# Kernel tuning notes

Hardware: AMD Instinct MI355X
Metric: run time of the kernel (lower is better)

The kernel has to match this reference:

```python
import math
import jax, jax.numpy as jnp
import numpy as np

B, S, D = 4, 2048, 1024
EPS_LN = 1e-5
EPS_MAS = 1e-9


def layernorm(x, g, b):
    m = jnp.mean(x, axis=-1, keepdims=True)
    v = jnp.mean(jnp.square(x - m), axis=-1, keepdims=True)
    return (x - m) * jax.lax.rsqrt(v + EPS_LN) * g + b


def spl(x, proto_w, mu_w, mu_b, gate):
    # match_values = x @ proto^T / sqrt(d);  comp = silu(x @ mu^T + b)
    match = jnp.einsum('bsd,od->bso', x, proto_w) / math.sqrt(x.shape[-1])
    comp = jax.nn.silu(jnp.einsum('bsd,od->bso', x, mu_w) + mu_b)
    return comp, match, gate


def branch(comp, match, gate, passthrough):
    # mas_normalize on the 1-D gate vector (cost), broadcast over [B,S,D]
    cost = gate / (jnp.max(jnp.abs(gate)) + EPS_MAS)
    rl = match - cost
    mrl = jax.nn.relu(rl)
    mask = (rl > 0).astype(comp.dtype)
    return comp * mrl + passthrough * (1.0 - mask)


def causal_attention(q, k, v):
    # num_heads = 1, head_dim = D, is_causal=True
    scale = 1.0 / math.sqrt(q.shape[-1])
    scores = jnp.einsum('bqd,bkd->bqk', q, k) * scale
    causal = jnp.tril(jnp.ones((q.shape[1], k.shape[1]), dtype=bool))
    scores = jnp.where(causal, scores, jnp.asarray(-1e9, scores.dtype))
    p = jax.nn.softmax(scores, axis=-1)
    return jnp.einsum('bqk,bkd->bqd', p, v)


def setup_inputs() -> dict:
    key = jax.random.key(0)
    ks = jax.random.split(key, 16)
    d = D
    std = 0.02
    inp = {
        'x': jax.random.normal(ks[0], (B, S, d), jnp.float32),
        'ln_g': jnp.ones((d,), jnp.float32),
        'ln_b': jnp.zeros((d,), jnp.float32),
    }
    names = ['q', 'k', 'v', 'o']
    for i, n in enumerate(names):
        inp[f'{n}_mu_w'] = std * jax.random.normal(ks[1 + 3 * i], (d, d), jnp.float32)
        inp[f'{n}_mu_b'] = jnp.zeros((d,), jnp.float32)
        inp[f'{n}_proto'] = std * jax.random.normal(ks[2 + 3 * i], (d, d), jnp.float32)
        inp[f'{n}_gate'] = 0.1 * jax.random.normal(ks[3 + 3 * i], (d,), jnp.float32)
    return inp


def reference(x, ln_g, ln_b,
              q_mu_w, q_mu_b, q_proto, q_gate,
              k_mu_w, k_mu_b, k_proto, k_gate,
              v_mu_w, v_mu_b, v_proto, v_gate,
              o_mu_w, o_mu_b, o_proto, o_gate):
    ln1_out = layernorm(x, ln_g, ln_b)

    c_q, mv_q, g_q = spl(ln1_out, q_proto, q_mu_w, q_mu_b, q_gate)
    c_k, mv_k, g_k = spl(ln1_out, k_proto, k_mu_w, k_mu_b, k_gate)
    c_v, mv_v, g_v = spl(ln1_out, v_proto, v_mu_w, v_mu_b, v_gate)

    q = branch(c_q, mv_q, g_q, ln1_out)
    k = branch(c_k, mv_k, g_k, ln1_out)
    v = branch(c_v, mv_v, g_v, ln1_out)

    attn_out = causal_attention(q, k, v)

    c_o, mv_o, g_o = spl(attn_out, o_proto, o_mu_w, o_mu_b, o_gate)
    masked_o = branch(c_o, mv_o, g_o, attn_out)

    x_out = x + masked_o
    return x_out
```

## Files before the change

### kernel.cpp

```cpp
#include <hip/hip_runtime.h>
#include <hip/hip_bf16.h>
#include <cmath>
#include <cstdint>

typedef _Float16 f16;
typedef _Float16 f16x8 __attribute__((ext_vector_type(8)));
typedef float f32x4 __attribute__((ext_vector_type(4)));

#define D_ 1024
#define S_ 2048


__device__ __forceinline__ void gload_lds16(const void* g, void* l) {
  __builtin_amdgcn_global_load_lds(
      (const __attribute__((address_space(1))) void*)(unsigned long long)(uintptr_t)g,
      (__attribute__((address_space(3))) void*)(unsigned int)(uintptr_t)l,
      16, 0, 0);
}

__device__ __forceinline__ int lds_off(int row, int cb) {
  return (row << 5) + ((cb ^ ((row >> 1) & 3)) << 3);
}

__device__ __forceinline__ void split1024(float v, f16& h, f16& l) {
  float s = v * 1024.f;
  h = (f16)s;
  l = (f16)(s - (float)h);
}

__device__ __forceinline__ void stage_tile(const f16* __restrict__ src, int ld,
                                           f16* lds, int wid, int lane) {
  const int r = (wid << 5) + (lane >> 2);
  const int c = (lane & 3) ^ ((r >> 1) & 3);
  const f16* g0 = src + (size_t)r * ld + (c << 3);
  gload_lds16(g0, lds + (wid << 10));
  gload_lds16(g0 + (size_t)(ld << 4), lds + (wid << 10) + 512);
}

__global__ __launch_bounds__(256) void convert_w(
    const float* __restrict__ s0, const float* __restrict__ s1,
    const float* __restrict__ s2, const float* __restrict__ s3,
    const float* __restrict__ s4, const float* __restrict__ s5,
    const float* __restrict__ s6, const float* __restrict__ s7,
    f16* __restrict__ dst) {
  const float* srcs[8] = {s0, s1, s2, s3, s4, s5, s6, s7};
  const float* sp = srcs[blockIdx.y];
  f16* hi = dst + (size_t)blockIdx.y * 2097152;
  f16* lo = hi + 1048576;
  const int i = (blockIdx.x * 256 + threadIdx.x) << 2;
  float4 f = *(const float4*)(sp + i);
  __align__(8) f16 h4[4], l4[4];
  split1024(f.x, h4[0], l4[0]); split1024(f.y, h4[1], l4[1]);
  split1024(f.z, h4[2], l4[2]); split1024(f.w, h4[3], l4[3]);
  *(uint2*)(hi + i) = *(uint2*)h4;
  *(uint2*)(lo + i) = *(uint2*)l4;
}

__global__ __launch_bounds__(256) void cost_k(
    const float* __restrict__ g0, const float* __restrict__ g1,
    const float* __restrict__ g2, const float* __restrict__ g3,
    float* __restrict__ cost) {
  const float* gp = blockIdx.x == 0 ? g0 : blockIdx.x == 1 ? g1
                   : blockIdx.x == 2 ? g2 : g3;
  const int t = threadIdx.x;
  float4 v = *(const float4*)(gp + (t << 2));
  float mx = fmaxf(fmaxf(fabsf(v.x), fabsf(v.y)), fmaxf(fabsf(v.z), fabsf(v.w)));
  for (int o = 32; o; o >>= 1) mx = fmaxf(mx, __shfl_xor(mx, o, 64));
  __shared__ float red[4];
  if ((t & 63) == 0) red[t >> 6] = mx;
  __syncthreads();
  mx = fmaxf(fmaxf(red[0], red[1]), fmaxf(red[2], red[3]));
  const float den = mx + 1e-9f;
  float4 o = {v.x / den, v.y / den, v.z / den, v.w / den};
  *(float4*)(cost + (blockIdx.x << 10) + (t << 2)) = o;
}

__global__ __launch_bounds__(256) void layernorm_k(
    const float* __restrict__ x, const float* __restrict__ g,
    const float* __restrict__ bta, f16* __restrict__ Lh, f16* __restrict__ Ll) {
  const int row = blockIdx.x, t = threadIdx.x;
  const float* xr = x + (size_t)row * D_;
  float4 v = *(const float4*)(xr + (t << 2));
  float s = v.x + v.y + v.z + v.w;
  float q = v.x * v.x + v.y * v.y + v.z * v.z + v.w * v.w;
  for (int o = 32; o; o >>= 1) { s += __shfl_xor(s, o, 64); q += __shfl_xor(q, o, 64); }
  __shared__ float red[8];
  const int wid = t >> 6;
  if ((t & 63) == 0) { red[wid] = s; red[4 + wid] = q; }
  __syncthreads();
  s = red[0] + red[1] + red[2] + red[3];
  q = red[4] + red[5] + red[6] + red[7];
  const float mean = s * (1.f / D_);
  const float var = q * (1.f / D_) - mean * mean;
  const float inv = 1.f / sqrtf(var + 1e-5f);
  float4 gv = *(const float4*)(g + (t << 2));
  float4 bv = *(const float4*)(bta + (t << 2));
  __align__(8) f16 h4[4], l4[4];
  split1024((v.x - mean) * inv * gv.x + bv.x, h4[0], l4[0]);
  split1024((v.y - mean) * inv * gv.y + bv.y, h4[1], l4[1]);
  split1024((v.z - mean) * inv * gv.z + bv.z, h4[2], l4[2]);
  split1024((v.w - mean) * inv * gv.w + bv.w, h4[3], l4[3]);
  const size_t off = (size_t)row * D_ + (t << 2);
  *(uint2*)(Lh + off) = *(uint2*)h4;
  *(uint2*)(Ll + off) = *(uint2*)l4;
}

#define MFMA16(a, b, c) __builtin_amdgcn_mfma_f32_16x16x32_f16((a), (b), (c), 0, 0, 0)

#define PH_CORE(N)                                                        \
    const f16x8 bph = *(const f16x8*)&bb[16384 + boff[N]];                \
    const f16x8 bpl = *(const f16x8*)&bb[20480 + boff[N]];                \
    const f16x8 bmh = *(const f16x8*)&bb[24576 + boff[N]];                \
    const f16x8 bml = *(const f16x8*)&bb[28672 + boff[N]];                \
    asm volatile("s_waitcnt lgkmcnt(0)" ::: "memory");                    \
    __builtin_amdgcn_sched_barrier(0);                                    \
    __builtin_amdgcn_s_setprio(1);                                        \
    _Pragma("unroll")                                                     \
    for (int m = 0; m < 4; ++m) {                                         \
      accP[m][N] = MFMA16(ah[m], bph, accP[m][N]);                        \
      accP[m][N] = MFMA16(ah[m], bpl, accP[m][N]);                        \
      accP[m][N] = MFMA16(al[m], bph, accP[m][N]);                        \
      accM[m][N] = MFMA16(ah[m], bmh, accM[m][N]);                        \
      accM[m][N] = MFMA16(ah[m], bml, accM[m][N]);                        \
      if (MUP == 3) accM[m][N] = MFMA16(al[m], bmh, accM[m][N]);          \
    }                                                                     \
    __builtin_amdgcn_s_setprio(0);                                        \
    asm volatile("s_barrier" ::: "memory");

#define DOPHASE_S(N, G0, L0, G1, L1)                                      \
  { gload_lds16((G0), (L0)); gload_lds16((G1), (L1)); PH_CORE(N) }

#define DOPHASE_N(N) { PH_CORE(N) }

template <int EPI, int MUP>
__global__ __launch_bounds__(512, 1) void dual_gemm_v3(
    const f16* __restrict__ Ah, const f16* __restrict__ Al,
    const f16* __restrict__ Wph, const f16* __restrict__ Wpl,
    const f16* __restrict__ Wmh, const f16* __restrict__ Wml,
    const float* __restrict__ bias, const float* __restrict__ cost,
    const f16* __restrict__ passh, const f16* __restrict__ passl,
    const float* __restrict__ xres, f16* __restrict__ outh,
    f16* __restrict__ outl, float* __restrict__ outf) {
  __shared__ __align__(16) f16 smem[65536];
  const int tid = threadIdx.x, wid = tid >> 6, lane = tid & 63;
  const int row0 = blockIdx.x << 8, col0 = blockIdx.y << 7;
  const int wr = (wid >> 1) << 6, wc = (wid & 1) << 6;
  const int arow = lane & 15, cbk = lane >> 4;

  const int sr = tid >> 2;
  const int sc = ((tid & 3) ^ ((sr >> 1) & 3)) << 3;
  const int wbase = wid << 9;

  const f16* pA0 = Ah + (size_t)(row0 + sr) * D_ + sc;
  const f16* pA1 = Ah + (size_t)(row0 + 128 + sr) * D_ + sc;
  const f16* pL0 = Al + (size_t)(row0 + sr) * D_ + sc;
  const f16* pL1 = Al + (size_t)(row0 + 128 + sr) * D_ + sc;
  const f16* pPh = Wph + (size_t)(col0 + sr) * D_ + sc;
  const f16* pPl = Wpl + (size_t)(col0 + sr) * D_ + sc;
  const f16* pMh = Wmh + (size_t)(col0 + sr) * D_ + sc;
  const f16* pMl = Wml + (size_t)(col0 + sr) * D_ + sc;

  const f32x4 zero = {0.f, 0.f, 0.f, 0.f};
  f32x4 accP[4][4], accM[4][4];
#pragma unroll
  for (int m = 0; m < 4; ++m)
#pragma unroll
    for (int n = 0; n < 4; ++n) { accP[m][n] = zero; accM[m][n] = zero; }

  int aoff[4], boff[4];
#pragma unroll
  for (int m = 0; m < 4; ++m) aoff[m] = lds_off(wr + m * 16 + arow, cbk);
#pragma unroll
  for (int n = 0; n < 4; ++n) boff[n] = lds_off(wc + n * 16 + arow, cbk);

  {
    f16* b = smem;
    gload_lds16(pA0, b + wbase);          gload_lds16(pA1, b + 4096 + wbase);
    gload_lds16(pL0, b + 8192 + wbase);   gload_lds16(pL1, b + 12288 + wbase);
    gload_lds16(pPh, b + 16384 + wbase);  gload_lds16(pPl, b + 20480 + wbase);
    gload_lds16(pMh, b + 24576 + wbase);  gload_lds16(pMl, b + 28672 + wbase);
  }

  int cur = 0;
  for (int t = 0; t < 32; ++t) {
    const f16* bb = smem + (cur << 15);
    f16* nb = smem + ((cur ^ 1) << 15);
    const int kn = (t < 31) ? ((t + 1) << 5) : 0;

    f16x8 ah[4], al[4];
    gload_lds16(pA0 + kn, nb + wbase);
    gload_lds16(pA1 + kn, nb + 4096 + wbase);
    asm volatile("s_waitcnt vmcnt(2)\n\ts_barrier" ::: "memory");
    __builtin_amdgcn_sched_barrier(0);
#pragma unroll
    for (int m = 0; m < 4; ++m) {
      ah[m] = *(const f16x8*)&bb[aoff[m]];
      al[m] = *(const f16x8*)&bb[8192 + aoff[m]];
    }
    DOPHASE_S(0, pL0 + kn, nb + 8192 + wbase, pL1 + kn, nb + 12288 + wbase)
    DOPHASE_S(1, pPh + kn, nb + 16384 + wbase, pPl + kn, nb + 20480 + wbase)
    DOPHASE_S(2, pMh + kn, nb + 24576 + wbase, pMl + kn, nb + 28672 + wbase)
    DOPHASE_N(3)
    cur ^= 1;
  }

#pragma unroll
  for (int m = 0; m < 4; ++m) {
    const int rb = row0 + wr + m * 16 + ((lane >> 4) << 2);
#pragma unroll
    for (int n = 0; n < 4; ++n) {
      const int col = col0 + wc + n * 16 + (lane & 15);
      const float cb2 = cost[col], bbv = bias[col];
#pragma unroll
      for (int j = 0; j < 4; ++j) {
        const size_t off = (size_t)(rb + j) * D_ + col;
        const float match = accP[m][n][j] * (1.f / 33554432.f);
        const float pre = accM[m][n][j] * (1.f / 1048576.f) + bbv;
        const float comp = pre / (1.f + expf(-pre));
        const float rl = match - cb2;
        float ov;
        if (rl > 0.f) ov = comp * rl;
        else ov = ((float)passh[off] + (float)passl[off]) * (1.f / 1024.f);
        if (EPI == 0) {
          f16 h, l; split1024(ov, h, l);
          outh[off] = h; outl[off] = l;
        } else {
          outf[off] = xres[off] + ov;
        }
      }
    }
  }
}

__global__ __launch_bounds__(256) void transpose_v(
    const f16* __restrict__ Vh, const f16* __restrict__ Vl,
    f16* __restrict__ VTh, f16* __restrict__ VTl) {
  const int iz = blockIdx.z, b = iz & 3;
  const f16* src = (iz >> 2) ? Vl : Vh;
  f16* dst = (iz >> 2) ? VTl : VTh;
  const int d0 = blockIdx.x << 6, s0 = blockIdx.y << 6;
  __shared__ f16 tl[64][65];
  const int c = threadIdx.x & 63, r4 = threadIdx.x >> 6;
  const f16* vb = src + (size_t)b * S_ * D_;
#pragma unroll
  for (int i = 0; i < 16; ++i) {
    const int sr = (r4 << 4) + i;
    tl[sr][c] = vb[(size_t)(s0 + sr) * D_ + d0 + c];
  }
  __syncthreads();
  f16* db = dst + (size_t)b * D_ * S_;
#pragma unroll
  for (int i = 0; i < 16; ++i) {
    const int dr = (r4 << 4) + i;
    db[(size_t)(d0 + dr) * S_ + s0 + c] = tl[c][dr];
  }
}

__global__ __launch_bounds__(256, 2) void scores_gemm(
    const f16* __restrict__ Qh, const f16* __restrict__ Ql,
    const f16* __restrict__ Kh, const f16* __restrict__ Kl,
    float* __restrict__ SC) {
  const int rt = blockIdx.x, ct = blockIdx.y, b = blockIdx.z;
  if (ct > rt) return;
  __shared__ __align__(16) f16 lQh[4096], lQl[4096], lKh[4096], lKl[4096];
  const int tid = threadIdx.x, wid = tid >> 6, lane = tid & 63;
  const int row0 = rt << 7, col0 = ct << 7;
  const int wr = (wid >> 1) << 6, wc = (wid & 1) << 6;
  const int arow = lane & 15, cb = lane >> 4;
  const f32x4 zero = {0.f, 0.f, 0.f, 0.f};
  f32x4 acc[4][4];
#pragma unroll
  for (int m = 0; m < 4; ++m)
#pragma unroll
    for (int n = 0; n < 4; ++n) acc[m][n] = zero;
  const f16* Qhb = Qh + ((size_t)b * S_ + row0) * D_;
  const f16* Qlb = Ql + ((size_t)b * S_ + row0) * D_;
  const f16* Khb = Kh + ((size_t)b * S_ + col0) * D_;
  const f16* Klb = Kl + ((size_t)b * S_ + col0) * D_;
  for (int k = 0; k < D_; k += 32) {
    stage_tile(Qhb + k, D_, lQh, wid, lane);
    stage_tile(Qlb + k, D_, lQl, wid, lane);
    stage_tile(Khb + k, D_, lKh, wid, lane);
    stage_tile(Klb + k, D_, lKl, wid, lane);
    __syncthreads();
    f16x8 bh[4], bl[4];
#pragma unroll
    for (int n = 0; n < 4; ++n) {
      const int bo = lds_off(wc + n * 16 + arow, cb);
      bh[n] = *(const f16x8*)&lKh[bo];
      bl[n] = *(const f16x8*)&lKl[bo];
    }
#pragma unroll
    for (int m = 0; m < 4; ++m) {
      const int ao = lds_off(wr + m * 16 + arow, cb);
      f16x8 ah = *(const f16x8*)&lQh[ao];
      f16x8 al = *(const f16x8*)&lQl[ao];
#pragma unroll
      for (int n = 0; n < 4; ++n) {
        acc[m][n] = __builtin_amdgcn_mfma_f32_16x16x32_f16(ah, bh[n], acc[m][n], 0, 0, 0);
        acc[m][n] = __builtin_amdgcn_mfma_f32_16x16x32_f16(ah, bl[n], acc[m][n], 0, 0, 0);
        acc[m][n] = __builtin_amdgcn_mfma_f32_16x16x32_f16(al, bh[n], acc[m][n], 0, 0, 0);
      }
    }
    __syncthreads();
  }
  float* scb = SC + (size_t)b * S_ * S_;
#pragma unroll
  for (int m = 0; m < 4; ++m) {
    const int rb = row0 + wr + m * 16 + ((lane >> 4) << 2);
#pragma unroll
    for (int n = 0; n < 4; ++n) {
      const int col = col0 + wc + n * 16 + (lane & 15);
#pragma unroll
      for (int j = 0; j < 4; ++j)
        scb[(size_t)(rb + j) * S_ + col] = acc[m][n][j] * (1.f / 33554432.f);
    }
  }
}

__global__ __launch_bounds__(256) void softmax_rows(float* __restrict__ SC) {
  const int r = blockIdx.x;
  const int s = r & 2047;
  float* rowf = SC + (size_t)r * S_;
  const int t = threadIdx.x, c0 = t << 3;
  float f[8];
  float4 u0 = *(const float4*)(rowf + c0);
  float4 u1 = *(const float4*)(rowf + c0 + 4);
  f[0] = u0.x; f[1] = u0.y; f[2] = u0.z; f[3] = u0.w;
  f[4] = u1.x; f[5] = u1.y; f[6] = u1.z; f[7] = u1.w;
  float mx = -3.0e38f;
#pragma unroll
  for (int j = 0; j < 8; ++j)
    if (c0 + j <= s) mx = fmaxf(mx, f[j]);
  for (int o = 32; o; o >>= 1) mx = fmaxf(mx, __shfl_xor(mx, o, 64));
  __shared__ float red[8];
  const int wid = t >> 6;
  if ((t & 63) == 0) red[wid] = mx;
  __syncthreads();
  mx = fmaxf(fmaxf(red[0], red[1]), fmaxf(red[2], red[3]));
  float e[8];
  float sum = 0.f;
#pragma unroll
  for (int j = 0; j < 8; ++j) {
    e[j] = (c0 + j <= s) ? expf(f[j] - mx) : 0.f;
    sum += e[j];
  }
  for (int o = 32; o; o >>= 1) sum += __shfl_xor(sum, o, 64);
  if ((t & 63) == 0) red[4 + wid] = sum;
  __syncthreads();
  sum = red[4] + red[5] + red[6] + red[7];
  f16* rowh = (f16*)rowf;
  __align__(16) f16 ph[8], pl[8];
#pragma unroll
  for (int j = 0; j < 8; ++j) {
    float p = (e[j] / sum) * 2048.f;
    ph[j] = (f16)p;
    pl[j] = (f16)(p - (float)ph[j]);
  }
  *(uint4*)(rowh + c0) = *(uint4*)ph;
  *(uint4*)(rowh + 2048 + c0) = *(uint4*)pl;
}

__global__ __launch_bounds__(256, 2) void pv_gemm(
    const f16* __restrict__ P, const f16* __restrict__ VTh,
    const f16* __restrict__ VTl, f16* __restrict__ Ath, f16* __restrict__ Atl) {
  const int rt = blockIdx.x, ct = blockIdx.y, b = blockIdx.z;
  __shared__ __align__(16) f16 lPh[4096], lPl[4096], lVh[4096], lVl[4096];
  const int tid = threadIdx.x, wid = tid >> 6, lane = tid & 63;
  const int row0 = rt << 7, col0 = ct << 7;
  const int wr = (wid >> 1) << 6, wc = (wid & 1) << 6;
  const int arow = lane & 15, cb = lane >> 4;
  const f32x4 zero = {0.f, 0.f, 0.f, 0.f};
  f32x4 acc[4][4];
#pragma unroll
  for (int m = 0; m < 4; ++m)
#pragma unroll
    for (int n = 0; n < 4; ++n) acc[m][n] = zero;
  const f16* Pb = P + ((size_t)b * S_ + row0) * 4096;
  const f16* Vhb = VTh + (size_t)b * D_ * S_ + (size_t)col0 * S_;
  const f16* Vlb = VTl + (size_t)b * D_ * S_ + (size_t)col0 * S_;
  const int kend = (rt + 1) << 7;
  for (int k = 0; k < kend; k += 32) {
    stage_tile(Pb + k, 4096, lPh, wid, lane);
    stage_tile(Pb + 2048 + k, 4096, lPl, wid, lane);
    stage_tile(Vhb + k, S_, lVh, wid, lane);
    stage_tile(Vlb + k, S_, lVl, wid, lane);
    __syncthreads();
    f16x8 bh[4], bl[4];
#pragma unroll
    for (int n = 0; n < 4; ++n) {
      const int bo = lds_off(wc + n * 16 + arow, cb);
      bh[n] = *(const f16x8*)&lVh[bo];
      bl[n] = *(const f16x8*)&lVl[bo];
    }
#pragma unroll
    for (int m = 0; m < 4; ++m) {
      const int ao = lds_off(wr + m * 16 + arow, cb);
      f16x8 ah = *(const f16x8*)&lPh[ao];
      f16x8 al = *(const f16x8*)&lPl[ao];
#pragma unroll
      for (int n = 0; n < 4; ++n) {
        acc[m][n] = __builtin_amdgcn_mfma_f32_16x16x32_f16(ah, bh[n], acc[m][n], 0, 0, 0);
        acc[m][n] = __builtin_amdgcn_mfma_f32_16x16x32_f16(ah, bl[n], acc[m][n], 0, 0, 0);
        acc[m][n] = __builtin_amdgcn_mfma_f32_16x16x32_f16(al, bh[n], acc[m][n], 0, 0, 0);
      }
    }
    __syncthreads();
  }
#pragma unroll
  for (int m = 0; m < 4; ++m) {
    const int rb = row0 + wr + m * 16 + ((lane >> 4) << 2);
#pragma unroll
    for (int n = 0; n < 4; ++n) {
      const int col = col0 + wc + n * 16 + (lane & 15);
#pragma unroll
      for (int j = 0; j < 4; ++j) {
        const float at = acc[m][n][j] * (1.f / 2097152.f);
        const size_t off = ((size_t)b * S_ + rb + j) * D_ + col;
        f16 h, l; split1024(at, h, l);
        Ath[off] = h; Atl[off] = l;
      }
    }
  }
}

extern "C" void kernel_launch(void* const* d_in, const int* in_sizes, int n_in,
                              void* d_out, int out_size, void* d_ws, size_t ws_size,
                              hipStream_t stream) {
  (void)in_sizes; (void)n_in; (void)out_size; (void)ws_size;
  const float* x      = (const float*)d_in[0];
  const float* ln_g   = (const float*)d_in[1];
  const float* ln_b   = (const float*)d_in[2];
  const float* q_mu_w = (const float*)d_in[3];
  const float* q_mu_b = (const float*)d_in[4];
  const float* q_pro  = (const float*)d_in[5];
  const float* q_gate = (const float*)d_in[6];
  const float* k_mu_w = (const float*)d_in[7];
  const float* k_mu_b = (const float*)d_in[8];
  const float* k_pro  = (const float*)d_in[9];
  const float* k_gate = (const float*)d_in[10];
  const float* v_mu_w = (const float*)d_in[11];
  const float* v_mu_b = (const float*)d_in[12];
  const float* v_pro  = (const float*)d_in[13];
  const float* v_gate = (const float*)d_in[14];
  const float* o_mu_w = (const float*)d_in[15];
  const float* o_mu_b = (const float*)d_in[16];
  const float* o_pro  = (const float*)d_in[17];
  const float* o_gate = (const float*)d_in[18];

  char* w = (char*)d_ws;
  f16* WB = (f16*)w;
  const size_t WS = 2097152;
  f16* Lh  = (f16*)(w + 33554432);
  f16* Ll  = (f16*)(w + 50331648);
  f16* Qh  = (f16*)(w + 67108864);
  f16* Ql  = (f16*)(w + 83886080);
  f16* Kh  = (f16*)(w + 100663296);
  f16* Kl  = (f16*)(w + 117440512);
  f16* VTh = (f16*)(w + 134217728);
  f16* VTl = (f16*)(w + 150994944);
  float* SC = (float*)(w + 167772160);
  float* COST = (float*)(w + 234881024);
  f16* Vh = (f16*)SC;
  f16* Vl = (f16*)(w + 184549376);
  f16* Ath = Qh;  f16* Atl = Ql;

  convert_w<<<dim3(1024, 8), 256, 0, stream>>>(
      q_pro, q_mu_w, k_pro, k_mu_w, v_pro, v_mu_w, o_pro, o_mu_w, WB);
  cost_k<<<4, 256, 0, stream>>>(q_gate, k_gate, v_gate, o_gate, COST);
  layernorm_k<<<8192, 256, 0, stream>>>(x, ln_g, ln_b, Lh, Ll);

  dual_gemm_v3<0, 3><<<dim3(32, 8), 512, 0, stream>>>(
      Lh, Ll, WB, WB + 1048576, WB + WS, WB + WS + 1048576,
      q_mu_b, COST, Lh, Ll, nullptr, Qh, Ql, nullptr);
  dual_gemm_v3<0, 3><<<dim3(32, 8), 512, 0, stream>>>(
      Lh, Ll, WB + 2 * WS, WB + 2 * WS + 1048576, WB + 3 * WS, WB + 3 * WS + 1048576,
      k_mu_b, COST + 1024, Lh, Ll, nullptr, Kh, Kl, nullptr);
  dual_gemm_v3<0, 3><<<dim3(32, 8), 512, 0, stream>>>(
      Lh, Ll, WB + 4 * WS, WB + 4 * WS + 1048576, WB + 5 * WS, WB + 5 * WS + 1048576,
      v_mu_b, COST + 2048, Lh, Ll, nullptr, Vh, Vl, nullptr);

  transpose_v<<<dim3(16, 32, 8), 256, 0, stream>>>(Vh, Vl, VTh, VTl);
  scores_gemm<<<dim3(16, 16, 4), 256, 0, stream>>>(Qh, Ql, Kh, Kl, SC);
  softmax_rows<<<8192, 256, 0, stream>>>(SC);
  pv_gemm<<<dim3(16, 8, 4), 256, 0, stream>>>((const f16*)SC, VTh, VTl, Ath, Atl);

  dual_gemm_v3<1, 2><<<dim3(32, 8), 512, 0, stream>>>(
      Ath, Atl, WB + 6 * WS, WB + 6 * WS + 1048576, WB + 7 * WS, WB + 7 * WS + 1048576,
      o_mu_b, COST + 3072, Ath, Atl, x, nullptr, nullptr, (float*)d_out);
}
```

Baseline: 678.9 us.

## Double-buffer B fragments in registers and drop per-phase barriers in dual GEMM

Restructures the dual GEMM main loop so B fragments for the next N sub-tile are read from LDS into registers while MFMAs for the current sub-tile run, using two alternating register sets. The four per-phase s_barrier / lgkmcnt(0) waits are replaced by a single vmcnt(0) plus barrier at the end of each k-iteration. MFMAs are regrouped into independent runs across m to lengthen the gap between dependent accumulator updates. In exchange, register pressure rises, and global prefetch for the next tile must now fully complete by the end of each iteration rather than being waited on partially.

```diff
diff --git a/kernel.cpp b/kernel.cpp
--- a/kernel.cpp
+++ b/kernel.cpp
@@ -107,33 +107,27 @@
 
 #define MFMA16(a, b, c) __builtin_amdgcn_mfma_f32_16x16x32_f16((a), (b), (c), 0, 0, 0)
 
-#define PH_CORE(N)                                                        \
-    const f16x8 bph = *(const f16x8*)&bb[16384 + boff[N]];                \
-    const f16x8 bpl = *(const f16x8*)&bb[20480 + boff[N]];                \
-    const f16x8 bmh = *(const f16x8*)&bb[24576 + boff[N]];                \
-    const f16x8 bml = *(const f16x8*)&bb[28672 + boff[N]];                \
-    asm volatile("s_waitcnt lgkmcnt(0)" ::: "memory");                    \
-    __builtin_amdgcn_sched_barrier(0);                                    \
-    __builtin_amdgcn_s_setprio(1);                                        \
-    _Pragma("unroll")                                                     \
-    for (int m = 0; m < 4; ++m) {                                         \
-      accP[m][N] = MFMA16(ah[m], bph, accP[m][N]);                        \
-      accP[m][N] = MFMA16(ah[m], bpl, accP[m][N]);                        \
-      accP[m][N] = MFMA16(al[m], bph, accP[m][N]);                        \
-      accM[m][N] = MFMA16(ah[m], bmh, accM[m][N]);                        \
-      accM[m][N] = MFMA16(ah[m], bml, accM[m][N]);                        \
-      if (MUP == 3) accM[m][N] = MFMA16(al[m], bmh, accM[m][N]);          \
-    }                                                                     \
-    __builtin_amdgcn_s_setprio(0);                                        \
-    asm volatile("s_barrier" ::: "memory");
-
-#define DOPHASE_S(N, G0, L0, G1, L1)                                      \
-  { gload_lds16((G0), (L0)); gload_lds16((G1), (L1)); PH_CORE(N) }
-
-#define DOPHASE_N(N) { PH_CORE(N) }
+#define MFMA_PHASE(N, BPH, BPL, BMH, BML)                                  \
+  __builtin_amdgcn_sched_barrier(0);                                       \
+  __builtin_amdgcn_s_setprio(1);                                           \
+  _Pragma("unroll") for (int m = 0; m < 4; ++m)                            \
+      accP[m][N] = MFMA16(ah[m], (BPH), accP[m][N]);                       \
+  _Pragma("unroll") for (int m = 0; m < 4; ++m)                            \
+      accP[m][N] = MFMA16(ah[m], (BPL), accP[m][N]);                       \
+  _Pragma("unroll") for (int m = 0; m < 4; ++m)                            \
+      accP[m][N] = MFMA16(al[m], (BPH), accP[m][N]);                       \
+  _Pragma("unroll") for (int m = 0; m < 4; ++m)                            \
+      accM[m][N] = MFMA16(ah[m], (BMH), accM[m][N]);                       \
+  _Pragma("unroll") for (int m = 0; m < 4; ++m)                            \
+      accM[m][N] = MFMA16(ah[m], (BML), accM[m][N]);                       \
+  if (MUP == 3) {                                                          \
+    _Pragma("unroll") for (int m = 0; m < 4; ++m)                          \
+        accM[m][N] = MFMA16(al[m], (BMH), accM[m][N]);                     \
+  }                                                                        \
+  __builtin_amdgcn_s_setprio(0);
 
 template <int EPI, int MUP>
-__global__ __launch_bounds__(512, 1) void dual_gemm_v3(
+__global__ __launch_bounds__(512, 1) void dual_gemm_v4(
     const f16* __restrict__ Ah, const f16* __restrict__ Al,
     const f16* __restrict__ Wph, const f16* __restrict__ Wpl,
     const f16* __restrict__ Wmh, const f16* __restrict__ Wml,
@@ -180,6 +174,9 @@
     gload_lds16(pPh, b + 16384 + wbase);  gload_lds16(pPl, b + 20480 + wbase);
     gload_lds16(pMh, b + 24576 + wbase);  gload_lds16(pMl, b + 28672 + wbase);
   }
+  asm volatile("s_waitcnt vmcnt(0)" ::: "memory");
+  __builtin_amdgcn_s_barrier();
+  __builtin_amdgcn_sched_barrier(0);
 
   int cur = 0;
   for (int t = 0; t < 32; ++t) {
@@ -188,19 +185,46 @@
     const int kn = (t < 31) ? ((t + 1) << 5) : 0;
 
     f16x8 ah[4], al[4];
-    gload_lds16(pA0 + kn, nb + wbase);
-    gload_lds16(pA1 + kn, nb + 4096 + wbase);
-    asm volatile("s_waitcnt vmcnt(2)\n\ts_barrier" ::: "memory");
-    __builtin_amdgcn_sched_barrier(0);
 #pragma unroll
     for (int m = 0; m < 4; ++m) {
       ah[m] = *(const f16x8*)&bb[aoff[m]];
       al[m] = *(const f16x8*)&bb[8192 + aoff[m]];
     }
-    DOPHASE_S(0, pL0 + kn, nb + 8192 + wbase, pL1 + kn, nb + 12288 + wbase)
-    DOPHASE_S(1, pPh + kn, nb + 16384 + wbase, pPl + kn, nb + 20480 + wbase)
-    DOPHASE_S(2, pMh + kn, nb + 24576 + wbase, pMl + kn, nb + 28672 + wbase)
-    DOPHASE_N(3)
+    f16x8 xph = *(const f16x8*)&bb[16384 + boff[0]];
+    f16x8 xpl = *(const f16x8*)&bb[20480 + boff[0]];
+    f16x8 xmh = *(const f16x8*)&bb[24576 + boff[0]];
+    f16x8 xml = *(const f16x8*)&bb[28672 + boff[0]];
+    f16x8 yph = *(const f16x8*)&bb[16384 + boff[1]];
+    f16x8 ypl = *(const f16x8*)&bb[20480 + boff[1]];
+    f16x8 ymh = *(const f16x8*)&bb[24576 + boff[1]];
+    f16x8 yml = *(const f16x8*)&bb[28672 + boff[1]];
+    gload_lds16(pA0 + kn, nb + wbase);
+    gload_lds16(pA1 + kn, nb + 4096 + wbase);
+    MFMA_PHASE(0, xph, xpl, xmh, xml)
+
+    xph = *(const f16x8*)&bb[16384 + boff[2]];
+    xpl = *(const f16x8*)&bb[20480 + boff[2]];
+    xmh = *(const f16x8*)&bb[24576 + boff[2]];
+    xml = *(const f16x8*)&bb[28672 + boff[2]];
+    gload_lds16(pL0 + kn, nb + 8192 + wbase);
+    gload_lds16(pL1 + kn, nb + 12288 + wbase);
+    MFMA_PHASE(1, yph, ypl, ymh, yml)
+
+    yph = *(const f16x8*)&bb[16384 + boff[3]];
+    ypl = *(const f16x8*)&bb[20480 + boff[3]];
+    ymh = *(const f16x8*)&bb[24576 + boff[3]];
+    yml = *(const f16x8*)&bb[28672 + boff[3]];
+    gload_lds16(pPh + kn, nb + 16384 + wbase);
+    gload_lds16(pPl + kn, nb + 20480 + wbase);
+    MFMA_PHASE(2, xph, xpl, xmh, xml)
+
+    gload_lds16(pMh + kn, nb + 24576 + wbase);
+    gload_lds16(pMl + kn, nb + 28672 + wbase);
+    MFMA_PHASE(3, yph, ypl, ymh, yml)
+
+    asm volatile("s_waitcnt vmcnt(0)" ::: "memory");
+    __builtin_amdgcn_s_barrier();
+    __builtin_amdgcn_sched_barrier(0);
     cur ^= 1;
   }
 
@@ -470,13 +494,13 @@
   cost_k<<<4, 256, 0, stream>>>(q_gate, k_gate, v_gate, o_gate, COST);
   layernorm_k<<<8192, 256, 0, stream>>>(x, ln_g, ln_b, Lh, Ll);
 
-  dual_gemm_v3<0, 3><<<dim3(32, 8), 512, 0, stream>>>(
+  dual_gemm_v4<0, 3><<<dim3(32, 8), 512, 0, stream>>>(
       Lh, Ll, WB, WB + 1048576, WB + WS, WB + WS + 1048576,
       q_mu_b, COST, Lh, Ll, nullptr, Qh, Ql, nullptr);
-  dual_gemm_v3<0, 3><<<dim3(32, 8), 512, 0, stream>>>(
+  dual_gemm_v4<0, 3><<<dim3(32, 8), 512, 0, stream>>>(
       Lh, Ll, WB + 2 * WS, WB + 2 * WS + 1048576, WB + 3 * WS, WB + 3 * WS + 1048576,
       k_mu_b, COST + 1024, Lh, Ll, nullptr, Kh, Kl, nullptr);
-  dual_gemm_v3<0, 3><<<dim3(32, 8), 512, 0, stream>>>(
+  dual_gemm_v4<0, 3><<<dim3(32, 8), 512, 0, stream>>>(
       Lh, Ll, WB + 4 * WS, WB + 4 * WS + 1048576, WB + 5 * WS, WB + 5 * WS + 1048576,
       v_mu_b, COST + 2048, Lh, Ll, nullptr, Vh, Vl, nullptr);
 
@@ -485,7 +509,7 @@
   softmax_rows<<<8192, 256, 0, stream>>>(SC);
   pv_gemm<<<dim3(16, 8, 4), 256, 0, stream>>>((const f16*)SC, VTh, VTl, Ath, Atl);
 
-  dual_gemm_v3<1, 2><<<dim3(32, 8), 512, 0, stream>>>(
+  dual_gemm_v4<1, 2><<<dim3(32, 8), 512, 0, stream>>>(
       Ath, Atl, WB + 6 * WS, WB + 6 * WS + 1048576, WB + 7 * WS, WB + 7 * WS + 1048576,
       o_mu_b, COST + 3072, Ath, Atl, x, nullptr, nullptr, (float*)d_out);
 }
```

Result: no change. 672.5 us (-1.0%).

## Double dual-GEMM block to 1024 threads with 4x4 wave grid and simplified pipeline

Applied to the files above, without the earlier changes.

The dual GEMM kernel now runs 16 waves per block instead of 8. Each wave computes a 64x32 tile rather than 64x64, so it holds half as many accumulators. The staged four-phase interleaving of global-to-LDS loads with MFMA phases is replaced by one bulk prefetch per k-step, followed by the full MFMA loop and a barrier. The aim is more latency hiding through extra waves and lower register pressure, at the cost of losing the fine-grained load/compute overlap and raising per-thread A-fragment loads relative to the compute done.

```diff
diff --git a/kernel.cpp b/kernel.cpp
--- a/kernel.cpp
+++ b/kernel.cpp
@@ -107,33 +107,8 @@
 
 #define MFMA16(a, b, c) __builtin_amdgcn_mfma_f32_16x16x32_f16((a), (b), (c), 0, 0, 0)
 
-#define PH_CORE(N)                                                        \
-    const f16x8 bph = *(const f16x8*)&bb[16384 + boff[N]];                \
-    const f16x8 bpl = *(const f16x8*)&bb[20480 + boff[N]];                \
-    const f16x8 bmh = *(const f16x8*)&bb[24576 + boff[N]];                \
-    const f16x8 bml = *(const f16x8*)&bb[28672 + boff[N]];                \
-    asm volatile("s_waitcnt lgkmcnt(0)" ::: "memory");                    \
-    __builtin_amdgcn_sched_barrier(0);                                    \
-    __builtin_amdgcn_s_setprio(1);                                        \
-    _Pragma("unroll")                                                     \
-    for (int m = 0; m < 4; ++m) {                                         \
-      accP[m][N] = MFMA16(ah[m], bph, accP[m][N]);                        \
-      accP[m][N] = MFMA16(ah[m], bpl, accP[m][N]);                        \
-      accP[m][N] = MFMA16(al[m], bph, accP[m][N]);                        \
-      accM[m][N] = MFMA16(ah[m], bmh, accM[m][N]);                        \
-      accM[m][N] = MFMA16(ah[m], bml, accM[m][N]);                        \
-      if (MUP == 3) accM[m][N] = MFMA16(al[m], bmh, accM[m][N]);          \
-    }                                                                     \
-    __builtin_amdgcn_s_setprio(0);                                        \
-    asm volatile("s_barrier" ::: "memory");
-
-#define DOPHASE_S(N, G0, L0, G1, L1)                                      \
-  { gload_lds16((G0), (L0)); gload_lds16((G1), (L1)); PH_CORE(N) }
-
-#define DOPHASE_N(N) { PH_CORE(N) }
-
 template <int EPI, int MUP>
-__global__ __launch_bounds__(512, 1) void dual_gemm_v3(
+__global__ __launch_bounds__(1024) void dual_gemm_v5(
     const f16* __restrict__ Ah, const f16* __restrict__ Al,
     const f16* __restrict__ Wph, const f16* __restrict__ Wpl,
     const f16* __restrict__ Wmh, const f16* __restrict__ Wml,
@@ -144,42 +119,41 @@
   __shared__ __align__(16) f16 smem[65536];
   const int tid = threadIdx.x, wid = tid >> 6, lane = tid & 63;
   const int row0 = blockIdx.x << 8, col0 = blockIdx.y << 7;
-  const int wr = (wid >> 1) << 6, wc = (wid & 1) << 6;
+  const int wr = (wid & 3) << 6;
+  const int wc = (wid >> 2) << 5;
   const int arow = lane & 15, cbk = lane >> 4;
 
-  const int sr = tid >> 2;
-  const int sc = ((tid & 3) ^ ((sr >> 1) & 3)) << 3;
-  const int wbase = wid << 9;
-
-  const f16* pA0 = Ah + (size_t)(row0 + sr) * D_ + sc;
-  const f16* pA1 = Ah + (size_t)(row0 + 128 + sr) * D_ + sc;
-  const f16* pL0 = Al + (size_t)(row0 + sr) * D_ + sc;
-  const f16* pL1 = Al + (size_t)(row0 + 128 + sr) * D_ + sc;
-  const f16* pPh = Wph + (size_t)(col0 + sr) * D_ + sc;
-  const f16* pPl = Wpl + (size_t)(col0 + sr) * D_ + sc;
-  const f16* pMh = Wmh + (size_t)(col0 + sr) * D_ + sc;
-  const f16* pMl = Wml + (size_t)(col0 + sr) * D_ + sc;
+  const int srow = tid >> 2;
+  const int scA = ((tid & 3) ^ ((srow >> 1) & 3)) << 3;
+  const int wrow = srow & 127;
+  const int scW = ((tid & 3) ^ ((wrow >> 1) & 3)) << 3;
+  const int wsel = tid >> 9;
+  const int dstA = wid << 9;
+  const int dstW = 16384 + (wid << 9);
+  const int dstW2 = 24576 + (wid << 9);
+
+  const f16* pAh = Ah + (size_t)(row0 + srow) * D_ + scA;
+  const f16* pAl = Al + (size_t)(row0 + srow) * D_ + scA;
+  const f16* pW1 = (wsel ? Wpl : Wph) + (size_t)(col0 + wrow) * D_ + scW;
+  const f16* pW2 = (wsel ? Wml : Wmh) + (size_t)(col0 + wrow) * D_ + scW;
 
   const f32x4 zero = {0.f, 0.f, 0.f, 0.f};
-  f32x4 accP[4][4], accM[4][4];
+  f32x4 accP[4][2], accM[4][2];
 #pragma unroll
   for (int m = 0; m < 4; ++m)
 #pragma unroll
-    for (int n = 0; n < 4; ++n) { accP[m][n] = zero; accM[m][n] = zero; }
-
-  int aoff[4], boff[4];
+    for (int n = 0; n < 2; ++n) { accP[m][n] = zero; accM[m][n] = zero; }
+
+  int aoff[4], boff[2];
 #pragma unroll
   for (int m = 0; m < 4; ++m) aoff[m] = lds_off(wr + m * 16 + arow, cbk);
 #pragma unroll
-  for (int n = 0; n < 4; ++n) boff[n] = lds_off(wc + n * 16 + arow, cbk);
-
-  {
-    f16* b = smem;
-    gload_lds16(pA0, b + wbase);          gload_lds16(pA1, b + 4096 + wbase);
-    gload_lds16(pL0, b + 8192 + wbase);   gload_lds16(pL1, b + 12288 + wbase);
-    gload_lds16(pPh, b + 16384 + wbase);  gload_lds16(pPl, b + 20480 + wbase);
-    gload_lds16(pMh, b + 24576 + wbase);  gload_lds16(pMl, b + 28672 + wbase);
-  }
+  for (int n = 0; n < 2; ++n) boff[n] = lds_off(wc + n * 16 + arow, cbk);
+
+  gload_lds16(pAh, smem + dstA);
+  gload_lds16(pAl, smem + 8192 + dstA);
+  gload_lds16(pW1, smem + dstW);
+  gload_lds16(pW2, smem + dstW2);
 
   int cur = 0;
   for (int t = 0; t < 32; ++t) {
@@ -187,20 +161,38 @@
     f16* nb = smem + ((cur ^ 1) << 15);
     const int kn = (t < 31) ? ((t + 1) << 5) : 0;
 
+    gload_lds16(pAh + kn, nb + dstA);
+    gload_lds16(pAl + kn, nb + 8192 + dstA);
+    gload_lds16(pW1 + kn, nb + dstW);
+    gload_lds16(pW2 + kn, nb + dstW2);
+    asm volatile("s_waitcnt vmcnt(4)\n\ts_barrier" ::: "memory");
+    __builtin_amdgcn_sched_barrier(0);
+
     f16x8 ah[4], al[4];
-    gload_lds16(pA0 + kn, nb + wbase);
-    gload_lds16(pA1 + kn, nb + 4096 + wbase);
-    asm volatile("s_waitcnt vmcnt(2)\n\ts_barrier" ::: "memory");
-    __builtin_amdgcn_sched_barrier(0);
 #pragma unroll
     for (int m = 0; m < 4; ++m) {
       ah[m] = *(const f16x8*)&bb[aoff[m]];
       al[m] = *(const f16x8*)&bb[8192 + aoff[m]];
     }
-    DOPHASE_S(0, pL0 + kn, nb + 8192 + wbase, pL1 + kn, nb + 12288 + wbase)
-    DOPHASE_S(1, pPh + kn, nb + 16384 + wbase, pPl + kn, nb + 20480 + wbase)
-    DOPHASE_S(2, pMh + kn, nb + 24576 + wbase, pMl + kn, nb + 28672 + wbase)
-    DOPHASE_N(3)
+    __builtin_amdgcn_s_setprio(1);
+#pragma unroll
+    for (int n = 0; n < 2; ++n) {
+      const f16x8 bph = *(const f16x8*)&bb[16384 + boff[n]];
+      const f16x8 bpl = *(const f16x8*)&bb[20480 + boff[n]];
+      const f16x8 bmh = *(const f16x8*)&bb[24576 + boff[n]];
+      const f16x8 bml = *(const f16x8*)&bb[28672 + boff[n]];
+#pragma unroll
+      for (int m = 0; m < 4; ++m) {
+        accP[m][n] = MFMA16(ah[m], bph, accP[m][n]);
+        accP[m][n] = MFMA16(ah[m], bpl, accP[m][n]);
+        accP[m][n] = MFMA16(al[m], bph, accP[m][n]);
+        accM[m][n] = MFMA16(ah[m], bmh, accM[m][n]);
+        accM[m][n] = MFMA16(ah[m], bml, accM[m][n]);
+        if (MUP == 3) accM[m][n] = MFMA16(al[m], bmh, accM[m][n]);
+      }
+    }
+    __builtin_amdgcn_s_setprio(0);
+    asm volatile("s_waitcnt lgkmcnt(0)\n\ts_barrier" ::: "memory");
     cur ^= 1;
   }
 
@@ -208,7 +200,7 @@
   for (int m = 0; m < 4; ++m) {
     const int rb = row0 + wr + m * 16 + ((lane >> 4) << 2);
 #pragma unroll
-    for (int n = 0; n < 4; ++n) {
+    for (int n = 0; n < 2; ++n) {
       const int col = col0 + wc + n * 16 + (lane & 15);
       const float cb2 = cost[col], bbv = bias[col];
 #pragma unroll
@@ -470,13 +462,13 @@
   cost_k<<<4, 256, 0, stream>>>(q_gate, k_gate, v_gate, o_gate, COST);
   layernorm_k<<<8192, 256, 0, stream>>>(x, ln_g, ln_b, Lh, Ll);
 
-  dual_gemm_v3<0, 3><<<dim3(32, 8), 512, 0, stream>>>(
+  dual_gemm_v5<0, 3><<<dim3(32, 8), 1024, 0, stream>>>(
       Lh, Ll, WB, WB + 1048576, WB + WS, WB + WS + 1048576,
       q_mu_b, COST, Lh, Ll, nullptr, Qh, Ql, nullptr);
-  dual_gemm_v3<0, 3><<<dim3(32, 8), 512, 0, stream>>>(
+  dual_gemm_v5<0, 3><<<dim3(32, 8), 1024, 0, stream>>>(
       Lh, Ll, WB + 2 * WS, WB + 2 * WS + 1048576, WB + 3 * WS, WB + 3 * WS + 1048576,
       k_mu_b, COST + 1024, Lh, Ll, nullptr, Kh, Kl, nullptr);
-  dual_gemm_v3<0, 3><<<dim3(32, 8), 512, 0, stream>>>(
+  dual_gemm_v5<0, 3><<<dim3(32, 8), 1024, 0, stream>>>(
       Lh, Ll, WB + 4 * WS, WB + 4 * WS + 1048576, WB + 5 * WS, WB + 5 * WS + 1048576,
       v_mu_b, COST + 2048, Lh, Ll, nullptr, Vh, Vl, nullptr);
 
@@ -485,7 +477,7 @@
   softmax_rows<<<8192, 256, 0, stream>>>(SC);
   pv_gemm<<<dim3(16, 8, 4), 256, 0, stream>>>((const f16*)SC, VTh, VTl, Ath, Atl);
 
-  dual_gemm_v3<1, 2><<<dim3(32, 8), 512, 0, stream>>>(
+  dual_gemm_v5<1, 2><<<dim3(32, 8), 1024, 0, stream>>>(
       Ath, Atl, WB + 6 * WS, WB + 6 * WS + 1048576, WB + 7 * WS, WB + 7 * WS + 1048576,
       o_mu_b, COST + 3072, Ath, Atl, x, nullptr, nullptr, (float*)d_out);
 }
```

After: 690.9 us. Within noise of the previous version (+1.8%).
